# Performance work log

Hardware: AMD Instinct MI355X
Metric: run time of the kernel (lower is better)

Reference implementation:

```python
import jax, jax.numpy as jnp
import numpy as np

B, N, H, D2 = 2, 2048, 16, 64


def setup_inputs() -> dict:
    key = jax.random.key(0)
    k1, k2, k3 = jax.random.split(key, 3)
    keys = jax.random.normal(k1, (B, N, H, D2), dtype=jnp.float32)
    queries = jax.random.normal(k2, (B, N, H, D2), dtype=jnp.float32)
    values = jax.random.normal(k3, (B, N, H, D2), dtype=jnp.float32)
    return {"keys": keys, "queries": queries, "values": values}


def reference(keys, queries, values):
    b, n, h, d2 = keys.shape
    # Faithful to the original: torch uses .reshape (NOT transpose) to go
    # (b, n, h, d2) -> (b, h, n, d2), a pure memory reinterpretation.
    q = queries.reshape(b, h, n, d2)
    k = keys.reshape(b, h, n, d2)
    v = values.reshape(b, h, n, d2)
    scale = 1.0 / (d2 ** 0.5)
    # [b, h, n, n] attention scores
    scores = jnp.einsum('bhqd,bhkd->bhqk', q, k) * scale
    # causal mask: upper triangle (diagonal=1) set to -inf
    causal = jnp.triu(jnp.ones((n, n), dtype=bool), k=1)
    scores = jnp.where(causal, -jnp.inf, scores)
    attn = jax.nn.softmax(scores, axis=-1)
    out = jnp.einsum('bhqk,bhkd->bhqd', attn, v)
    return out.reshape(b, n, h, d2)
```

## Files before the change

kernel.cpp:

```cpp
#include <hip/hip_runtime.h>


typedef short  short8v __attribute__((ext_vector_type(8)));
typedef float  float8v __attribute__((ext_vector_type(8)));
typedef float  f32x16  __attribute__((ext_vector_type(16)));

#define NQ 2048
#define DD 64
#define KT 64
#define KP 72
#define VP 72

#define Z16 ((f32x16){0.f,0.f,0.f,0.f,0.f,0.f,0.f,0.f,0.f,0.f,0.f,0.f,0.f,0.f,0.f,0.f})
#define mfma32 __builtin_amdgcn_mfma_f32_32x32x16_bf16

union U4 { unsigned int u[4]; short8v s; };

static __device__ __forceinline__ unsigned int pktr(float lo, float hi) {
    return __builtin_amdgcn_perm(__builtin_bit_cast(unsigned int, hi),
                                 __builtin_bit_cast(unsigned int, lo),
                                 0x07060302);
}
static __device__ __forceinline__ unsigned int pkrn(float lo, float hi) {
    unsigned int a = __builtin_bit_cast(unsigned int, hi) + 0x8000u;
    unsigned int b = __builtin_bit_cast(unsigned int, lo) + 0x8000u;
    return __builtin_amdgcn_perm(a, b, 0x07060302);
}
static __device__ __forceinline__ unsigned int cvtpk(float lo, float hi) {
    unsigned int d;
    asm("v_cvt_pk_bf16_f32 %0, %1, %2" : "=v"(d) : "v"(lo), "v"(hi));
    return d;
}
static __device__ __forceinline__ float fexp2(float x) {
    float y;
    asm("v_exp_f32 %0, %1" : "=v"(y) : "v"(x));
    return y;
}

#define MK_PA(dst, S, B)                                                     \
    {                                                                        \
        unsigned int P0 = cvtpk(S[(B) + 0], S[(B) + 1]);                     \
        unsigned int P1 = cvtpk(S[(B) + 2], S[(B) + 3]);                     \
        unsigned int P2 = cvtpk(S[(B) + 4], S[(B) + 5]);                     \
        unsigned int P3 = cvtpk(S[(B) + 6], S[(B) + 7]);                     \
        asm("v_permlane32_swap_b32 %0, %1" : "+v"(P0), "+v"(P2));            \
        asm("v_permlane32_swap_b32 %0, %1" : "+v"(P1), "+v"(P3));            \
        U4 w_;                                                               \
        w_.u[0] = P0; w_.u[1] = P1; w_.u[2] = P2; w_.u[3] = P3;              \
        dst = w_.s;                                                          \
    }

#define VF(td, s) (*(const short8v*)&Vt[cur][((td) * 32 + q31) * VP + (s) * 16 + h * 8])

__global__ __launch_bounds__(256, 2) void mha_fwd_kernel(
    const float* __restrict__ Kg,
    const float* __restrict__ Qg,
    const float* __restrict__ Vg,
    float* __restrict__ Og)
{
    __shared__ __align__(16) unsigned short Klds[2][KT * KP];
    __shared__ __align__(16) unsigned short Vt[2][DD * VP];

    const int t    = threadIdx.x;
    const int lane = t & 63;
    const int wave = t >> 6;
    const int q31  = lane & 31;
    const int h    = lane >> 5;

    const int b   = blockIdx.x;
    const int rb  = b & 255;
    const int bh  = rb & 31;
    const int jj  = rb >> 5;
    const int Tq  = (b >> 8) ? jj : (15 - jj);
    const int nt  = 2 * Tq + 2;
    const int q0  = Tq * 128 + wave * 32;
    const int itl = 2 * Tq + (wave >> 1);

    const size_t base = (size_t)bh * NQ * DD;
    const float* Qp = Qg + base;
    const float* Kp = Kg + base;
    const float* Vp = Vg + base;
    float*       Op = Og + base;

    const float sscale = 0.125f * 1.4426950408889634f;

    const int kr = t >> 3, kc = (t & 7) * 8;
    const int vd = t & 63, vg = (t >> 6) * 16;

    short8v qf[4];
#pragma unroll
    for (int s = 0; s < 4; ++s) {
        float8v a = *(const float8v*)(Qp + (size_t)(q0 + q31) * DD + s * 16 + h * 8);
        U4 w;
#pragma unroll
        for (int i = 0; i < 4; ++i)
            w.u[i] = pkrn(a[2 * i] * sscale, a[2 * i + 1] * sscale);
        qf[s] = w.s;
    }

    float  l_i = 0.0f;
    f32x16 o0 = Z16, o1 = Z16;

    float8v ka0, ka1;
    float   vr[16];

    {
        ka0 = *(const float8v*)(Kp + (size_t)kr * DD + kc);
        ka1 = *(const float8v*)(Kp + (size_t)(kr + 32) * DD + kc);
#pragma unroll
        for (int i = 0; i < 16; ++i)
            vr[i] = Vp[(size_t)(vg + i) * DD + vd];
        U4 w0, w1, wv0, wv1;
#pragma unroll
        for (int i = 0; i < 4; ++i) {
            w0.u[i]  = pktr(ka0[2 * i], ka0[2 * i + 1]);
            w1.u[i]  = pktr(ka1[2 * i], ka1[2 * i + 1]);
            wv0.u[i] = pktr(vr[2 * i], vr[2 * i + 1]);
            wv1.u[i] = pktr(vr[8 + 2 * i], vr[9 + 2 * i]);
        }
        *(short8v*)&Klds[0][kr * KP + kc]        = w0.s;
        *(short8v*)&Klds[0][(kr + 32) * KP + kc] = w1.s;
        *(short8v*)&Vt[0][vd * VP + vg]          = wv0.s;
        *(short8v*)&Vt[0][vd * VP + vg + 8]      = wv1.s;
    }
    __syncthreads();

    for (int it = 0; it < nt; ++it) {
        const int  cur = it & 1;
        const bool stg = (it + 1 < nt);

        if (stg) {
            const int nkb = (it + 1) * KT;
            ka0 = *(const float8v*)(Kp + (size_t)(nkb + kr) * DD + kc);
            ka1 = *(const float8v*)(Kp + (size_t)(nkb + kr + 32) * DD + kc);
#pragma unroll
            for (int i = 0; i < 16; ++i)
                vr[i] = Vp[(size_t)(nkb + vg + i) * DD + vd];
        }
        __builtin_amdgcn_sched_barrier(0);

        if (it <= itl) {
            __builtin_amdgcn_s_setprio(1);
            const bool diag = (it == itl);
            const bool do1  = (!diag) || (wave & 1);

            short8v pa0, pa1, pa2, pa3;

            {
                f32x16 sT = Z16;
#pragma unroll
                for (int s = 0; s < 4; ++s) {
                    short8v kf = *(const short8v*)&Klds[cur][q31 * KP + s * 16 + h * 8];
                    sT = mfma32(kf, qf[s], sT, 0, 0, 0);
                }
                if (diag && !(wave & 1)) {
#pragma unroll
                    for (int r = 0; r < 16; ++r) {
                        const int kcst = (r & 3) + 8 * (r >> 2);
                        if (kcst + 4 * h > q31) sT[r] = -3.0e38f;
                    }
                }
#pragma unroll
                for (int r = 0; r < 16; ++r) sT[r] = fexp2(sT[r]);
                l_i += (((sT[0] + sT[1]) + (sT[2] + sT[3])) +
                        ((sT[4] + sT[5]) + (sT[6] + sT[7]))) +
                       (((sT[8] + sT[9]) + (sT[10] + sT[11])) +
                        ((sT[12] + sT[13]) + (sT[14] + sT[15])));
                MK_PA(pa0, sT, 0);
                MK_PA(pa1, sT, 8);
            }
            o0 = mfma32(pa0, VF(0, 0), o0, 0, 0, 0);
            o1 = mfma32(pa0, VF(1, 0), o1, 0, 0, 0);
            o0 = mfma32(pa1, VF(0, 1), o0, 0, 0, 0);
            o1 = mfma32(pa1, VF(1, 1), o1, 0, 0, 0);

            if (do1) {
                f32x16 sU = Z16;
#pragma unroll
                for (int s = 0; s < 4; ++s) {
                    short8v kf = *(const short8v*)&Klds[cur][(32 + q31) * KP + s * 16 + h * 8];
                    sU = mfma32(kf, qf[s], sU, 0, 0, 0);
                }
                if (diag && (wave & 1)) {
#pragma unroll
                    for (int r = 0; r < 16; ++r) {
                        const int kcst = (r & 3) + 8 * (r >> 2);
                        if (kcst + 4 * h > q31) sU[r] = -3.0e38f;
                    }
                }
#pragma unroll
                for (int r = 0; r < 16; ++r) sU[r] = fexp2(sU[r]);
                l_i += (((sU[0] + sU[1]) + (sU[2] + sU[3])) +
                        ((sU[4] + sU[5]) + (sU[6] + sU[7]))) +
                       (((sU[8] + sU[9]) + (sU[10] + sU[11])) +
                        ((sU[12] + sU[13]) + (sU[14] + sU[15])));
                MK_PA(pa2, sU, 0);
                MK_PA(pa3, sU, 8);
                o0 = mfma32(pa2, VF(0, 2), o0, 0, 0, 0);
                o1 = mfma32(pa2, VF(1, 2), o1, 0, 0, 0);
                o0 = mfma32(pa3, VF(0, 3), o0, 0, 0, 0);
                o1 = mfma32(pa3, VF(1, 3), o1, 0, 0, 0);
            }
            __builtin_amdgcn_s_setprio(0);
        }

        if (stg) {
            U4 w0, w1, wv0, wv1;
#pragma unroll
            for (int i = 0; i < 4; ++i) {
                w0.u[i]  = pktr(ka0[2 * i], ka0[2 * i + 1]);
                w1.u[i]  = pktr(ka1[2 * i], ka1[2 * i + 1]);
                wv0.u[i] = pktr(vr[2 * i], vr[2 * i + 1]);
                wv1.u[i] = pktr(vr[8 + 2 * i], vr[9 + 2 * i]);
            }
            *(short8v*)&Klds[cur ^ 1][kr * KP + kc]        = w0.s;
            *(short8v*)&Klds[cur ^ 1][(kr + 32) * KP + kc] = w1.s;
            *(short8v*)&Vt[cur ^ 1][vd * VP + vg]          = wv0.s;
            *(short8v*)&Vt[cur ^ 1][vd * VP + vg + 8]      = wv1.s;
        }

        __syncthreads();
    }

    const float rs   = l_i + __shfl_xor(l_i, 32);
    const float rinv = 1.0f / rs;
#pragma unroll
    for (int r = 0; r < 16; ++r) {
        const int   qrow = (r & 3) + 8 * (r >> 2) + 4 * h;
        const float lv   = __shfl(rinv, qrow, 64);
        Op[(size_t)(q0 + qrow) * DD + q31]      = o0[r] * lv;
        Op[(size_t)(q0 + qrow) * DD + 32 + q31] = o1[r] * lv;
    }
}

extern "C" void kernel_launch(void* const* d_in, const int* in_sizes, int n_in,
                              void* d_out, int out_size, void* d_ws, size_t ws_size,
                              hipStream_t stream) {
    const float* keys    = (const float*)d_in[0];
    const float* queries = (const float*)d_in[1];
    const float* values  = (const float*)d_in[2];
    float* out           = (float*)d_out;

    dim3 grid(512);
    dim3 block(256, 1, 1);
    mha_fwd_kernel<<<grid, block, 0, stream>>>(keys, queries, values, out);
}
```

Before: 116.6 us.

## Warp-specialize attention: producer waves stage K/V, consumers split key halves

Grows each block from 4 to 10 waves: two producer waves load and convert the next K/V tile to bf16 in LDS, and eight consumer waves compute. Each consumer wave handles one 32-row query slice and one 32-key half of the tile, and the two halves' partial outputs and row sums are combined through LDS at the end. The aim is to take global-load latency and conversion off the compute waves and to spread the MFMA work over more waves. In exchange it adds an LDS reduction with an extra barrier, idle producer waves during compute, and a different occupancy profile.

```diff
diff --git a/kernel.cpp b/kernel.cpp
--- a/kernel.cpp
+++ b/kernel.cpp
@@ -50,16 +50,15 @@
         dst = w_.s;                                                          \
     }
 
-#define VF(td, s) (*(const short8v*)&Vt[cur][((td) * 32 + q31) * VP + (s) * 16 + h * 8])
-
-__global__ __launch_bounds__(256, 2) void mha_fwd_kernel(
+__global__ __launch_bounds__(640, 5) void mha_fwd_kernel(
     const float* __restrict__ Kg,
     const float* __restrict__ Qg,
     const float* __restrict__ Vg,
     float* __restrict__ Og)
 {
-    __shared__ __align__(16) unsigned short Klds[2][KT * KP];
-    __shared__ __align__(16) unsigned short Vt[2][DD * VP];
+    __shared__ __align__(16) unsigned short SM[2 * KT * KP + 2 * DD * VP];
+#define KL(c) (&SM[(c) * (KT * KP)])
+#define VT(c) (&SM[2 * (KT * KP) + (c) * (DD * VP)])
 
     const int t    = threadIdx.x;
     const int lane = t & 63;
@@ -73,8 +72,13 @@
     const int jj  = rb >> 5;
     const int Tq  = (b >> 8) ? jj : (15 - jj);
     const int nt  = 2 * Tq + 2;
-    const int q0  = Tq * 128 + wave * 32;
-    const int itl = 2 * Tq + (wave >> 1);
+
+    const bool producer = (wave >= 8);
+    const int  qw = wave & 3;
+    const int  kh = (wave >> 2) & 1;
+    const int  q0 = Tq * 128 + qw * 32;
+    const int  itl  = producer ? -1 : (2 * Tq + ((qw - kh) >> 1));
+    const bool hasd = !producer && (((qw - kh) & 1) == 0);
 
     const size_t base = (size_t)bh * NQ * DD;
     const float* Qp = Qg + base;
@@ -84,153 +88,154 @@
 
     const float sscale = 0.125f * 1.4426950408889634f;
 
-    const int kr = t >> 3, kc = (t & 7) * 8;
-    const int vd = t & 63, vg = (t >> 6) * 16;
+    const int pt = t - 512;
+    const int kr = pt >> 1, kc = (pt & 1) * 32;
+    const int vd = pt & 63, vg = ((pt >> 6) & 1) * 32;
 
     short8v qf[4];
-#pragma unroll
-    for (int s = 0; s < 4; ++s) {
-        float8v a = *(const float8v*)(Qp + (size_t)(q0 + q31) * DD + s * 16 + h * 8);
-        U4 w;
-#pragma unroll
-        for (int i = 0; i < 4; ++i)
-            w.u[i] = pkrn(a[2 * i] * sscale, a[2 * i + 1] * sscale);
-        qf[s] = w.s;
+    if (!producer) {
+#pragma unroll
+        for (int s = 0; s < 4; ++s) {
+            float8v a = *(const float8v*)(Qp + (size_t)(q0 + q31) * DD + s * 16 + h * 8);
+            U4 w;
+#pragma unroll
+            for (int i = 0; i < 4; ++i)
+                w.u[i] = pkrn(a[2 * i] * sscale, a[2 * i + 1] * sscale);
+            qf[s] = w.s;
+        }
     }
 
     float  l_i = 0.0f;
     f32x16 o0 = Z16, o1 = Z16;
 
-    float8v ka0, ka1;
-    float   vr[16];
-
-    {
-        ka0 = *(const float8v*)(Kp + (size_t)kr * DD + kc);
-        ka1 = *(const float8v*)(Kp + (size_t)(kr + 32) * DD + kc);
-#pragma unroll
-        for (int i = 0; i < 16; ++i)
+    if (producer) {
+        float8v ka[4];
+        float   vr[32];
+#pragma unroll
+        for (int i = 0; i < 4; ++i)
+            ka[i] = *(const float8v*)(Kp + (size_t)kr * DD + kc + i * 8);
+#pragma unroll
+        for (int i = 0; i < 32; ++i)
             vr[i] = Vp[(size_t)(vg + i) * DD + vd];
-        U4 w0, w1, wv0, wv1;
+        U4 w;
 #pragma unroll
         for (int i = 0; i < 4; ++i) {
-            w0.u[i]  = pktr(ka0[2 * i], ka0[2 * i + 1]);
-            w1.u[i]  = pktr(ka1[2 * i], ka1[2 * i + 1]);
-            wv0.u[i] = pktr(vr[2 * i], vr[2 * i + 1]);
-            wv1.u[i] = pktr(vr[8 + 2 * i], vr[9 + 2 * i]);
-        }
-        *(short8v*)&Klds[0][kr * KP + kc]        = w0.s;
-        *(short8v*)&Klds[0][(kr + 32) * KP + kc] = w1.s;
-        *(short8v*)&Vt[0][vd * VP + vg]          = wv0.s;
-        *(short8v*)&Vt[0][vd * VP + vg + 8]      = wv1.s;
+#pragma unroll
+            for (int jx = 0; jx < 4; ++jx)
+                w.u[jx] = pktr(ka[i][2 * jx], ka[i][2 * jx + 1]);
+            *(short8v*)&KL(0)[kr * KP + kc + i * 8] = w.s;
+        }
+#pragma unroll
+        for (int i = 0; i < 4; ++i) {
+#pragma unroll
+            for (int jx = 0; jx < 4; ++jx)
+                w.u[jx] = pktr(vr[8 * i + 2 * jx], vr[8 * i + 2 * jx + 1]);
+            *(short8v*)&VT(0)[vd * VP + vg + i * 8] = w.s;
+        }
     }
     __syncthreads();
 
     for (int it = 0; it < nt; ++it) {
-        const int  cur = it & 1;
-        const bool stg = (it + 1 < nt);
-
-        if (stg) {
-            const int nkb = (it + 1) * KT;
-            ka0 = *(const float8v*)(Kp + (size_t)(nkb + kr) * DD + kc);
-            ka1 = *(const float8v*)(Kp + (size_t)(nkb + kr + 32) * DD + kc);
-#pragma unroll
-            for (int i = 0; i < 16; ++i)
-                vr[i] = Vp[(size_t)(nkb + vg + i) * DD + vd];
-        }
-        __builtin_amdgcn_sched_barrier(0);
-
-        if (it <= itl) {
+        const int cur = it & 1;
+
+        if (producer) {
+            if (it + 1 < nt) {
+                const int nkb = (it + 1) * KT;
+                float8v ka[4];
+                float   vr[32];
+#pragma unroll
+                for (int i = 0; i < 4; ++i)
+                    ka[i] = *(const float8v*)(Kp + (size_t)(nkb + kr) * DD + kc + i * 8);
+#pragma unroll
+                for (int i = 0; i < 32; ++i)
+                    vr[i] = Vp[(size_t)(nkb + vg + i) * DD + vd];
+                U4 w;
+#pragma unroll
+                for (int i = 0; i < 4; ++i) {
+#pragma unroll
+                    for (int jx = 0; jx < 4; ++jx)
+                        w.u[jx] = pktr(ka[i][2 * jx], ka[i][2 * jx + 1]);
+                    *(short8v*)&KL(cur ^ 1)[kr * KP + kc + i * 8] = w.s;
+                }
+#pragma unroll
+                for (int i = 0; i < 4; ++i) {
+#pragma unroll
+                    for (int jx = 0; jx < 4; ++jx)
+                        w.u[jx] = pktr(vr[8 * i + 2 * jx], vr[8 * i + 2 * jx + 1]);
+                    *(short8v*)&VT(cur ^ 1)[vd * VP + vg + i * 8] = w.s;
+                }
+            }
+        } else if (it <= itl) {
             __builtin_amdgcn_s_setprio(1);
-            const bool diag = (it == itl);
-            const bool do1  = (!diag) || (wave & 1);
-
-            short8v pa0, pa1, pa2, pa3;
-
-            {
-                f32x16 sT = Z16;
-#pragma unroll
-                for (int s = 0; s < 4; ++s) {
-                    short8v kf = *(const short8v*)&Klds[cur][q31 * KP + s * 16 + h * 8];
-                    sT = mfma32(kf, qf[s], sT, 0, 0, 0);
+
+            f32x16 sT = Z16;
+#pragma unroll
+            for (int s = 0; s < 4; ++s) {
+                short8v kf = *(const short8v*)&KL(cur)[(kh * 32 + q31) * KP + s * 16 + h * 8];
+                sT = mfma32(kf, qf[s], sT, 0, 0, 0);
+            }
+
+            if (hasd && it == itl) {
+#pragma unroll
+                for (int r = 0; r < 16; ++r) {
+                    const int kcst = (r & 3) + 8 * (r >> 2);
+                    if (kcst + 4 * h > q31) sT[r] = -3.0e38f;
                 }
-                if (diag && !(wave & 1)) {
-#pragma unroll
-                    for (int r = 0; r < 16; ++r) {
-                        const int kcst = (r & 3) + 8 * (r >> 2);
-                        if (kcst + 4 * h > q31) sT[r] = -3.0e38f;
-                    }
-                }
-#pragma unroll
-                for (int r = 0; r < 16; ++r) sT[r] = fexp2(sT[r]);
-                l_i += (((sT[0] + sT[1]) + (sT[2] + sT[3])) +
-                        ((sT[4] + sT[5]) + (sT[6] + sT[7]))) +
-                       (((sT[8] + sT[9]) + (sT[10] + sT[11])) +
-                        ((sT[12] + sT[13]) + (sT[14] + sT[15])));
-                MK_PA(pa0, sT, 0);
-                MK_PA(pa1, sT, 8);
             }
-            o0 = mfma32(pa0, VF(0, 0), o0, 0, 0, 0);
-            o1 = mfma32(pa0, VF(1, 0), o1, 0, 0, 0);
-            o0 = mfma32(pa1, VF(0, 1), o0, 0, 0, 0);
-            o1 = mfma32(pa1, VF(1, 1), o1, 0, 0, 0);
-
-            if (do1) {
-                f32x16 sU = Z16;
-#pragma unroll
-                for (int s = 0; s < 4; ++s) {
-                    short8v kf = *(const short8v*)&Klds[cur][(32 + q31) * KP + s * 16 + h * 8];
-                    sU = mfma32(kf, qf[s], sU, 0, 0, 0);
-                }
-                if (diag && (wave & 1)) {
-#pragma unroll
-                    for (int r = 0; r < 16; ++r) {
-                        const int kcst = (r & 3) + 8 * (r >> 2);
-                        if (kcst + 4 * h > q31) sU[r] = -3.0e38f;
-                    }
-                }
-#pragma unroll
-                for (int r = 0; r < 16; ++r) sU[r] = fexp2(sU[r]);
-                l_i += (((sU[0] + sU[1]) + (sU[2] + sU[3])) +
-                        ((sU[4] + sU[5]) + (sU[6] + sU[7]))) +
-                       (((sU[8] + sU[9]) + (sU[10] + sU[11])) +
-                        ((sU[12] + sU[13]) + (sU[14] + sU[15])));
-                MK_PA(pa2, sU, 0);
-                MK_PA(pa3, sU, 8);
-                o0 = mfma32(pa2, VF(0, 2), o0, 0, 0, 0);
-                o1 = mfma32(pa2, VF(1, 2), o1, 0, 0, 0);
-                o0 = mfma32(pa3, VF(0, 3), o0, 0, 0, 0);
-                o1 = mfma32(pa3, VF(1, 3), o1, 0, 0, 0);
-            }
+
+#pragma unroll
+            for (int r = 0; r < 16; ++r) sT[r] = fexp2(sT[r]);
+            l_i += (((sT[0] + sT[1]) + (sT[2] + sT[3])) +
+                    ((sT[4] + sT[5]) + (sT[6] + sT[7]))) +
+                   (((sT[8] + sT[9]) + (sT[10] + sT[11])) +
+                    ((sT[12] + sT[13]) + (sT[14] + sT[15])));
+
+            short8v pa0, pa1;
+            MK_PA(pa0, sT, 0);
+            MK_PA(pa1, sT, 8);
+
+            const unsigned short* vb = VT(cur);
+            short8v v00 = *(const short8v*)&vb[q31 * VP        + (2 * kh)     * 16 + h * 8];
+            short8v v01 = *(const short8v*)&vb[q31 * VP        + (2 * kh + 1) * 16 + h * 8];
+            short8v v10 = *(const short8v*)&vb[(32 + q31) * VP + (2 * kh)     * 16 + h * 8];
+            short8v v11 = *(const short8v*)&vb[(32 + q31) * VP + (2 * kh + 1) * 16 + h * 8];
+            o0 = mfma32(pa0, v00, o0, 0, 0, 0);
+            o0 = mfma32(pa1, v01, o0, 0, 0, 0);
+            o1 = mfma32(pa0, v10, o1, 0, 0, 0);
+            o1 = mfma32(pa1, v11, o1, 0, 0, 0);
+
             __builtin_amdgcn_s_setprio(0);
         }
 
-        if (stg) {
-            U4 w0, w1, wv0, wv1;
-#pragma unroll
-            for (int i = 0; i < 4; ++i) {
-                w0.u[i]  = pktr(ka0[2 * i], ka0[2 * i + 1]);
-                w1.u[i]  = pktr(ka1[2 * i], ka1[2 * i + 1]);
-                wv0.u[i] = pktr(vr[2 * i], vr[2 * i + 1]);
-                wv1.u[i] = pktr(vr[8 + 2 * i], vr[9 + 2 * i]);
-            }
-            *(short8v*)&Klds[cur ^ 1][kr * KP + kc]        = w0.s;
-            *(short8v*)&Klds[cur ^ 1][(kr + 32) * KP + kc] = w1.s;
-            *(short8v*)&Vt[cur ^ 1][vd * VP + vg]          = wv0.s;
-            *(short8v*)&Vt[cur ^ 1][vd * VP + vg + 8]      = wv1.s;
-        }
-
         __syncthreads();
     }
 
-    const float rs   = l_i + __shfl_xor(l_i, 32);
-    const float rinv = 1.0f / rs;
-#pragma unroll
-    for (int r = 0; r < 16; ++r) {
-        const int   qrow = (r & 3) + 8 * (r >> 2) + 4 * h;
-        const float lv   = __shfl(rinv, qrow, 64);
-        Op[(size_t)(q0 + qrow) * DD + q31]      = o0[r] * lv;
-        Op[(size_t)(q0 + qrow) * DD + 32 + q31] = o1[r] * lv;
-    }
+    const float rs0 = l_i + __shfl_xor(l_i, 32);
+    float* smf = (float*)SM;
+    if (!producer && kh == 1) {
+        float* dst = smf + (qw * 64 + lane) * 33;
+#pragma unroll
+        for (int r = 0; r < 16; ++r) { dst[r] = o0[r]; dst[16 + r] = o1[r]; }
+        dst[32] = rs0;
+    }
+    __syncthreads();
+    if (!producer && kh == 0) {
+        const float* src = smf + (qw * 64 + lane) * 33;
+        float rs = rs0 + src[32];
+        f32x16 f0 = o0, f1 = o1;
+#pragma unroll
+        for (int r = 0; r < 16; ++r) { f0[r] += src[r]; f1[r] += src[16 + r]; }
+        const float rinv = 1.0f / rs;
+#pragma unroll
+        for (int r = 0; r < 16; ++r) {
+            const int   qrow = (r & 3) + 8 * (r >> 2) + 4 * h;
+            const float lv   = __shfl(rinv, qrow, 64);
+            Op[(size_t)(q0 + qrow) * DD + q31]      = f0[r] * lv;
+            Op[(size_t)(q0 + qrow) * DD + 32 + q31] = f1[r] * lv;
+        }
+    }
+#undef KL
+#undef VT
 }
 
 extern "C" void kernel_launch(void* const* d_in, const int* in_sizes, int n_in,
@@ -242,6 +247,6 @@
     float* out           = (float*)d_out;
 
     dim3 grid(512);
-    dim3 block(256, 1, 1);
+    dim3 block(640, 1, 1);
     mha_fwd_kernel<<<grid, block, 0, stream>>>(keys, queries, values, out);
 }
```

Measured after the change: 267.1 us. 2.29x slower.

## Split long causal query tiles across two blocks and merge with combine kernel

Applied to the files above, without the earlier changes.

For query tiles in the upper half of the sequence, the key range is split in two and handled by separate blocks that write unnormalized partial outputs and row sums to workspace. A second kernel adds the two halves and normalizes them. The aim is to balance the causal workload across 768 blocks so the longest blocks no longer set the tail latency. In exchange it adds workspace traffic, a second launch, and drops a scheduling barrier in the main loop. The split appears to rely on no running max being kept, so the two partial sums can simply be added.

```diff
diff --git a/kernel.cpp b/kernel.cpp
--- a/kernel.cpp
+++ b/kernel.cpp
@@ -2,6 +2,7 @@
 
 
 typedef short  short8v __attribute__((ext_vector_type(8)));
+typedef float  float4v __attribute__((ext_vector_type(4)));
 typedef float  float8v __attribute__((ext_vector_type(8)));
 typedef float  f32x16  __attribute__((ext_vector_type(16)));
 
@@ -10,6 +11,7 @@
 #define KT 64
 #define KP 72
 #define VP 72
+#define SLOT 8320
 
 #define Z16 ((f32x16){0.f,0.f,0.f,0.f,0.f,0.f,0.f,0.f,0.f,0.f,0.f,0.f,0.f,0.f,0.f,0.f})
 #define mfma32 __builtin_amdgcn_mfma_f32_32x32x16_bf16
@@ -56,7 +58,9 @@
     const float* __restrict__ Kg,
     const float* __restrict__ Qg,
     const float* __restrict__ Vg,
-    float* __restrict__ Og)
+    float* __restrict__ Og,
+    float* __restrict__ ws,
+    const int mode)
 {
     __shared__ __align__(16) unsigned short Klds[2][KT * KP];
     __shared__ __align__(16) unsigned short Vt[2][DD * VP];
@@ -67,12 +71,37 @@
     const int q31  = lane & 31;
     const int h    = lane >> 5;
 
-    const int b   = blockIdx.x;
-    const int rb  = b & 255;
-    const int bh  = rb & 31;
-    const int jj  = rb >> 5;
-    const int Tq  = (b >> 8) ? jj : (15 - jj);
-    const int nt  = 2 * Tq + 2;
+    int bh, Tq, it0, it1;
+    bool partial;
+    float* wp = nullptr;
+    const int b = blockIdx.x;
+    if (mode == 0) {
+        const int rb = b & 255;
+        bh = rb & 31;
+        const int jj = rb >> 5;
+        Tq = (b >> 8) ? jj : (15 - jj);
+        it0 = 0; it1 = 2 * Tq + 2;
+        partial = false;
+    } else {
+        const int reg = b >> 8;
+        const int rb  = b & 255;
+        bh = rb & 31;
+        const int jj = rb >> 5;
+        if (reg == 2) {
+            Tq = 7 - jj;
+            it0 = 0; it1 = 2 * Tq + 2;
+            partial = false;
+        } else {
+            Tq = 15 - jj;
+            const int slot = bh * 8 + (Tq - 8);
+            if (reg == 0) { it0 = Tq + 1; it1 = 2 * Tq + 2;
+                            wp = ws + (size_t)(256 + slot) * SLOT; }
+            else          { it0 = 0;      it1 = Tq + 1;
+                            wp = ws + (size_t)slot * SLOT; }
+            partial = true;
+        }
+    }
+
     const int q0  = Tq * 128 + wave * 32;
     const int itl = 2 * Tq + (wave >> 1);
 
@@ -101,34 +130,36 @@
     float  l_i = 0.0f;
     f32x16 o0 = Z16, o1 = Z16;
 
-    float8v ka0, ka1;
-    float   vr[16];
-
     {
-        ka0 = *(const float8v*)(Kp + (size_t)kr * DD + kc);
-        ka1 = *(const float8v*)(Kp + (size_t)(kr + 32) * DD + kc);
+        const int kb0 = it0 * KT;
+        const int pb  = it0 & 1;
+        float8v pka0 = *(const float8v*)(Kp + (size_t)(kb0 + kr) * DD + kc);
+        float8v pka1 = *(const float8v*)(Kp + (size_t)(kb0 + kr + 32) * DD + kc);
+        float pvr[16];
 #pragma unroll
         for (int i = 0; i < 16; ++i)
-            vr[i] = Vp[(size_t)(vg + i) * DD + vd];
+            pvr[i] = Vp[(size_t)(kb0 + vg + i) * DD + vd];
         U4 w0, w1, wv0, wv1;
 #pragma unroll
         for (int i = 0; i < 4; ++i) {
-            w0.u[i]  = pktr(ka0[2 * i], ka0[2 * i + 1]);
-            w1.u[i]  = pktr(ka1[2 * i], ka1[2 * i + 1]);
-            wv0.u[i] = pktr(vr[2 * i], vr[2 * i + 1]);
-            wv1.u[i] = pktr(vr[8 + 2 * i], vr[9 + 2 * i]);
-        }
-        *(short8v*)&Klds[0][kr * KP + kc]        = w0.s;
-        *(short8v*)&Klds[0][(kr + 32) * KP + kc] = w1.s;
-        *(short8v*)&Vt[0][vd * VP + vg]          = wv0.s;
-        *(short8v*)&Vt[0][vd * VP + vg + 8]      = wv1.s;
+            w0.u[i]  = pktr(pka0[2 * i], pka0[2 * i + 1]);
+            w1.u[i]  = pktr(pka1[2 * i], pka1[2 * i + 1]);
+            wv0.u[i] = pktr(pvr[2 * i], pvr[2 * i + 1]);
+            wv1.u[i] = pktr(pvr[8 + 2 * i], pvr[9 + 2 * i]);
+        }
+        *(short8v*)&Klds[pb][kr * KP + kc]        = w0.s;
+        *(short8v*)&Klds[pb][(kr + 32) * KP + kc] = w1.s;
+        *(short8v*)&Vt[pb][vd * VP + vg]          = wv0.s;
+        *(short8v*)&Vt[pb][vd * VP + vg + 8]      = wv1.s;
     }
     __syncthreads();
 
-    for (int it = 0; it < nt; ++it) {
+    for (int it = it0; it < it1; ++it) {
         const int  cur = it & 1;
-        const bool stg = (it + 1 < nt);
-
+        const bool stg = (it + 1 < it1);
+
+        float8v ka0, ka1;
+        float   vr[16];
         if (stg) {
             const int nkb = (it + 1) * KT;
             ka0 = *(const float8v*)(Kp + (size_t)(nkb + kr) * DD + kc);
@@ -137,7 +168,6 @@
             for (int i = 0; i < 16; ++i)
                 vr[i] = Vp[(size_t)(nkb + vg + i) * DD + vd];
         }
-        __builtin_amdgcn_sched_barrier(0);
 
         if (it <= itl) {
             __builtin_amdgcn_s_setprio(1);
@@ -222,14 +252,55 @@
         __syncthreads();
     }
 
-    const float rs   = l_i + __shfl_xor(l_i, 32);
-    const float rinv = 1.0f / rs;
-#pragma unroll
-    for (int r = 0; r < 16; ++r) {
-        const int   qrow = (r & 3) + 8 * (r >> 2) + 4 * h;
-        const float lv   = __shfl(rinv, qrow, 64);
-        Op[(size_t)(q0 + qrow) * DD + q31]      = o0[r] * lv;
-        Op[(size_t)(q0 + qrow) * DD + 32 + q31] = o1[r] * lv;
+    const float rs = l_i + __shfl_xor(l_i, 32);
+    if (partial) {
+        float* wl = wp;
+        float* wo = wp + 128;
+        if (h == 0) wl[wave * 32 + q31] = rs;
+#pragma unroll
+        for (int r = 0; r < 16; ++r) {
+            const int qrow = (r & 3) + 8 * (r >> 2) + 4 * h;
+            wo[(size_t)(wave * 32 + qrow) * DD + q31]      = o0[r];
+            wo[(size_t)(wave * 32 + qrow) * DD + 32 + q31] = o1[r];
+        }
+    } else {
+        const float rinv = 1.0f / rs;
+#pragma unroll
+        for (int r = 0; r < 16; ++r) {
+            const int   qrow = (r & 3) + 8 * (r >> 2) + 4 * h;
+            const float lv   = __shfl(rinv, qrow, 64);
+            Op[(size_t)(q0 + qrow) * DD + q31]      = o0[r] * lv;
+            Op[(size_t)(q0 + qrow) * DD + 32 + q31] = o1[r] * lv;
+        }
+    }
+}
+
+__global__ __launch_bounds__(256, 8) void mha_combine_kernel(
+    const float* __restrict__ ws,
+    float* __restrict__ Og)
+{
+    const int s  = blockIdx.x;
+    const int bh = s >> 3;
+    const int Tq = 8 + (s & 7);
+    const float* A = ws + (size_t)s * SLOT;
+    const float* B = ws + (size_t)(256 + s) * SLOT;
+
+    const int t   = threadIdx.x;
+    const int row = t >> 1;
+    const int ch  = (t & 1) * 32;
+
+    const float inv = 1.0f / (A[row] + B[row]);
+    const float* a = A + 128 + (size_t)row * DD + ch;
+    const float* b = B + 128 + (size_t)row * DD + ch;
+    float* op = Og + ((size_t)bh * NQ + Tq * 128 + row) * DD + ch;
+#pragma unroll
+    for (int i = 0; i < 8; ++i) {
+        float4v va = *(const float4v*)(a + i * 4);
+        float4v vb = *(const float4v*)(b + i * 4);
+        float4v vo;
+#pragma unroll
+        for (int j = 0; j < 4; ++j) vo[j] = (va[j] + vb[j]) * inv;
+        *(float4v*)(op + i * 4) = vo;
     }
 }
 
@@ -240,8 +311,15 @@
     const float* queries = (const float*)d_in[1];
     const float* values  = (const float*)d_in[2];
     float* out           = (float*)d_out;
-
-    dim3 grid(512);
-    dim3 block(256, 1, 1);
-    mha_fwd_kernel<<<grid, block, 0, stream>>>(keys, queries, values, out);
-}
+    float* ws            = (float*)d_ws;
+
+    const size_t need = (size_t)512 * SLOT * sizeof(float);
+    if (ws != nullptr && ws_size >= need) {
+        mha_fwd_kernel<<<dim3(768), dim3(256), 0, stream>>>(
+            keys, queries, values, out, ws, 1);
+        mha_combine_kernel<<<dim3(256), dim3(256), 0, stream>>>(ws, out);
+    } else {
+        mha_fwd_kernel<<<dim3(512), dim3(256), 0, stream>>>(
+            keys, queries, values, out, ws, 0);
+    }
+}
```

Result: slower. 129.6 us (+11.2%).
